# Performance work log

Hardware: AMD Instinct MI355X
Metric: run time of the kernel (lower is better)

Reference implementation:

```python
import jax, jax.numpy as jnp
import numpy as np

WS = 7          # window size
NUM_HEADS = 4
DIM = 128


def setup_inputs() -> dict:
    key = jax.random.key(0)
    k1, k2, k3, k4, k5 = jax.random.split(key, 5)
    B, H, W, C = 16, 112, 112, DIM
    x = jax.random.normal(k1, (B, H, W, C), dtype=jnp.float32)
    w_qkv = jax.random.normal(k2, (C, 3 * C), dtype=jnp.float32) * 0.02
    b_qkv = jax.random.normal(k3, (3 * C,), dtype=jnp.float32) * 0.02
    w_proj = jax.random.normal(k4, (C, C), dtype=jnp.float32) * 0.02
    b_proj = jax.random.normal(k5, (C,), dtype=jnp.float32) * 0.02
    return {"x": x, "w_qkv": w_qkv, "b_qkv": b_qkv, "w_proj": w_proj, "b_proj": b_proj}


def reference(x, w_qkv, b_qkv, w_proj, b_proj):
    B, H, W, C = x.shape
    nh, hd = NUM_HEADS, C // NUM_HEADS
    scale = hd ** (-0.5)
    pad_h = (WS - H % WS) % WS
    pad_w = (WS - W % WS) % WS
    if pad_h > 0 or pad_w > 0:
        x = jnp.pad(x, ((0, 0), (0, pad_h), (0, pad_w), (0, 0)))
    Hp, Wp = H + pad_h, W + pad_w
    nH, nW = Hp // WS, Wp // WS
    # window partition: [B,Hp,Wp,C] -> [B*nH*nW, WS*WS, C]
    win = x.reshape(B, nH, WS, nW, WS, C).transpose(0, 1, 3, 2, 4, 5)
    win = win.reshape(-1, WS * WS, C)
    nwin, N = win.shape[0], WS * WS
    qkv = win @ w_qkv + b_qkv                       # [nwin, N, 3C]
    qkv = qkv.reshape(nwin, N, 3, nh, hd).transpose(2, 0, 3, 1, 4)  # [3, nwin, nh, N, hd]
    q, k, v = qkv[0], qkv[1], qkv[2]
    attn = jnp.einsum("whnd,whmd->whnm", q, k) * scale
    attn = jax.nn.softmax(attn, axis=-1)
    out = jnp.einsum("whnm,whmd->whnd", attn, v)    # [nwin, nh, N, hd]
    out = out.transpose(0, 2, 1, 3).reshape(nwin, N, C)
    out = out @ w_proj + b_proj
    # window merge: [nwin, N, C] -> [B, Hp, Wp, C]
    out = out.reshape(B, nH, nW, WS, WS, C).transpose(0, 1, 3, 2, 4, 5)
    out = out.reshape(B, Hp, Wp, C)
    if pad_h > 0 or pad_w > 0:
        out = out[:, :H, :W, :]
    return out
```

## Files before the change

kernel.cpp:

```cpp
#include <hip/hip_runtime.h>
#include <hip/hip_bf16.h>

typedef short bf16x8 __attribute__((ext_vector_type(8)));
typedef short bf16x4 __attribute__((ext_vector_type(4)));
typedef float f32x4 __attribute__((ext_vector_type(4)));
typedef unsigned short ushort8v __attribute__((ext_vector_type(8)));

#define TPB 512

__device__ __forceinline__ unsigned short f2bf(float f) {
  __hip_bfloat16 h = __float2bfloat16(f);
  return __builtin_bit_cast(unsigned short, h);
}

__device__ __forceinline__ bf16x4 pack4(float a, float b, float c, float d) {
  bf16x4 v;
  v[0] = (short)f2bf(a); v[1] = (short)f2bf(b);
  v[2] = (short)f2bf(c); v[3] = (short)f2bf(d);
  return v;
}

__device__ __forceinline__ f32x4 mfma16(bf16x4 a, bf16x4 b, f32x4 c) {
#if __has_builtin(__builtin_amdgcn_mfma_f32_16x16x16_bf16)
  return __builtin_amdgcn_mfma_f32_16x16x16_bf16(a, b, c, 0, 0, 0);
#elif __has_builtin(__builtin_amdgcn_mfma_f32_16x16x16bf16_1k)
  return __builtin_amdgcn_mfma_f32_16x16x16bf16_1k(a, b, c, 0, 0, 0);
#else
  f32x4 d;
  asm("v_mfma_f32_16x16x16_bf16 %0, %1, %2, %3" : "=v"(d) : "v"(a), "v"(b), "v"(c));
  return d;
#endif
}

__device__ __forceinline__ float exp2_raw(float x) {
#if __has_builtin(__builtin_amdgcn_exp2f)
  return __builtin_amdgcn_exp2f(x);
#else
  float r; asm("v_exp_f32 %0, %1" : "=v"(r) : "v"(x)); return r;
#endif
}
__device__ __forceinline__ float rcp_raw(float x) {
#if __has_builtin(__builtin_amdgcn_rcpf)
  return __builtin_amdgcn_rcpf(x);
#else
  float r; asm("v_rcp_f32 %0, %1" : "=v"(r) : "v"(x)); return r;
#endif
}

#define Q_OFF   0
#define K_OFF   10240
#define ATT_OFF 0
#define VT_OFF  20480
#define SMEM_ELEMS 29696

#define CQ 0.25501817f

__global__ void prep_weights(const float* __restrict__ wqkv,
                             const float* __restrict__ wproj,
                             unsigned short* __restrict__ wt) {
  int idx = blockIdx.x * 256 + threadIdx.x;
  if (idx < 384 * 128) {
    int n = idx >> 7, k = idx & 127;
    wt[idx] = f2bf(wqkv[k * 384 + n]);
  } else if (idx < 384 * 128 + 128 * 128) {
    int j = idx - 384 * 128;
    int c = j >> 7, k = j & 127;
    wt[idx] = f2bf(wproj[k * 128 + c]);
  }
}

__launch_bounds__(TPB, 2)
__global__ void win_attn(const float* __restrict__ x,
                         const float* __restrict__ bqkv,
                         const float* __restrict__ bproj,
                         const unsigned short* __restrict__ wt,
                         float* __restrict__ out) {
  __shared__ __align__(16) unsigned short smem[SMEM_ELEMS];
  const int tid  = threadIdx.x;
  const int wave = tid >> 6;
  const int lane = tid & 63;
  const int g    = lane >> 4;
  const int l15  = lane & 15;

  const int wid = blockIdx.x;
  const int b = wid >> 8, wh = (wid >> 4) & 15, ww = wid & 15;
  const size_t winbase = (((size_t)b * 112 + wh * 7) * 112 + ww * 7) * 128;

  const unsigned short* wqkvT  = wt;
  const unsigned short* wprojT = wt + 384 * 128;

  bf16x4 idQ = {0, 0, 0, 0}, idK = {0, 0, 0, 0};
  if ((l15 >> 2) == g) {
    idQ[l15 & 3] = (short)f2bf(CQ);
    idK[l15 & 3] = (short)0x3F80;
  }

  for (int q = tid; q < 1024; q += TPB) {
    int row = q >> 4, c8 = q & 15;
    int rowc = min(row, 48);
    const float4* src = (const float4*)(x + winbase + ((rowc / 7) * 112 + (rowc % 7)) * 128 + c8 * 8);
    float4 f0 = src[0], f1 = src[1];
    ushort8v v8;
    v8[0] = f2bf(f0.x); v8[1] = f2bf(f0.y); v8[2] = f2bf(f0.z); v8[3] = f2bf(f0.w);
    v8[4] = f2bf(f1.x); v8[5] = f2bf(f1.y); v8[6] = f2bf(f1.z); v8[7] = f2bf(f1.w);
    int dst = row * 128 + ((c8 * 8) ^ ((row & 7) << 3));
    *(ushort8v*)(&smem[dst]) = v8;
  }
  __syncthreads();

  bf16x8 af[4][4];
#pragma unroll
  for (int mt = 0; mt < 4; mt++)
#pragma unroll
    for (int kt = 0; kt < 4; kt++) {
      int row = mt * 16 + l15;
      int colE = kt * 32 + g * 8;
      af[mt][kt] = *(const bf16x8*)(&smem[row * 128 + (colE ^ ((row & 7) << 3))]);
    }
  __syncthreads();

  const f32x4 zero4 = {0.f, 0.f, 0.f, 0.f};

#pragma unroll
  for (int i = 0; i < 3; i++) {
    int nt = wave * 3 + i;
    int n  = nt * 16 + l15;
    float bias = bqkv[n];
    f32x4 binit = {bias, bias, bias, bias};

    bf16x8 bw[4];
#pragma unroll
    for (int kt = 0; kt < 4; kt++)
      bw[kt] = *(const bf16x8*)(wqkvT + n * 128 + kt * 32 + g * 8);

    f32x4 acc[4] = {binit, binit, binit, binit};
    __builtin_amdgcn_s_setprio(1);
#pragma unroll
    for (int kt = 0; kt < 4; kt++)
#pragma unroll
      for (int mt = 0; mt < 4; mt++)
        acc[mt] = __builtin_amdgcn_mfma_f32_16x16x32_bf16(af[mt][kt], bw[kt], acc[mt], 0, 0, 0);
    __builtin_amdgcn_s_setprio(0);

    int sec = nt >> 3;
    if (sec == 2) {
      int hn = n & 127, h = hn >> 5, d = hn & 31;
#pragma unroll
      for (int mt = 0; mt < 4; mt++) {
        bf16x4 pv = pack4(acc[mt][0], acc[mt][1], acc[mt][2], acc[mt][3]);
        *(bf16x4*)(&smem[VT_OFF + h * 2304 + d * 72 + mt * 16 + g * 4]) = pv;
      }
    } else {
      int t7 = nt & 7;
      int hh = t7 >> 1, d0 = (t7 & 1) * 16;
      const bf16x4 idf = (sec == 0) ? idQ : idK;
      const int base = (sec == 0 ? Q_OFF : K_OFF) + hh * 2560 + d0 + g * 4;
#pragma unroll
      for (int mt = 0; mt < 4; mt++) {
        bf16x4 ax = pack4(acc[mt][0], acc[mt][1], acc[mt][2], acc[mt][3]);
        f32x4 dt = mfma16(ax, idf, zero4);
        bf16x4 w = pack4(dt[0], dt[1], dt[2], dt[3]);
        *(bf16x4*)(&smem[base + (mt * 16 + l15) * 40]) = w;
      }
    }
  }
  __syncthreads();

  const int h    = wave >> 1;
  const int half = wave & 1;

  bf16x8 ak[4];
#pragma unroll
  for (int kt = 0; kt < 4; kt++) {
    int row = kt * 16 + l15;
    ak[kt] = *(const bf16x8*)(&smem[K_OFF + h * 2560 + row * 40 + g * 8]);
  }
  bf16x8 bq[2];
#pragma unroll
  for (int qt = 0; qt < 2; qt++) {
    int row = half * 32 + qt * 16 + l15;
    bq[qt] = *(const bf16x8*)(&smem[Q_OFF + h * 2560 + row * 40 + g * 8]);
  }
  bf16x4 bv16[2][4];
#pragma unroll
  for (int nt2 = 0; nt2 < 2; nt2++)
#pragma unroll
    for (int kt = 0; kt < 4; kt++)
      bv16[nt2][kt] = *(const bf16x4*)(&smem[VT_OFF + h * 2304 + (nt2 * 16 + l15) * 72 + kt * 16 + g * 4]);

  f32x4 s[4][2];
  __builtin_amdgcn_s_setprio(1);
#pragma unroll
  for (int kt = 0; kt < 4; kt++)
#pragma unroll
    for (int qt = 0; qt < 2; qt++)
      s[kt][qt] = __builtin_amdgcn_mfma_f32_16x16x32_bf16(ak[kt], bq[qt], zero4, 0, 0, 0);
  __builtin_amdgcn_s_setprio(0);

  bf16x4 ap16[2][4];
  const bool v48 = (g == 0);
#pragma unroll
  for (int qt = 0; qt < 2; qt++) {
    float sum = 0.f;
#pragma unroll
    for (int kt = 0; kt < 3; kt++)
#pragma unroll
      for (int r = 0; r < 4; r++) {
        float p = exp2_raw(s[kt][qt][r]);
        s[kt][qt][r] = p;
        sum += p;
      }
    float p3 = v48 ? exp2_raw(s[3][qt][0]) : 0.0f;
    sum += p3;
    sum += __shfl_xor(sum, 16);
    sum += __shfl_xor(sum, 32);
    float inv = rcp_raw(sum);
#pragma unroll
    for (int kt = 0; kt < 3; kt++)
      ap16[qt][kt] = pack4(s[kt][qt][0] * inv, s[kt][qt][1] * inv,
                           s[kt][qt][2] * inv, s[kt][qt][3] * inv);
    ap16[qt][3] = pack4(p3 * inv, 0.f, 0.f, 0.f);
  }

  f32x4 o[2][2] = {{zero4, zero4}, {zero4, zero4}};
  __builtin_amdgcn_s_setprio(1);
#pragma unroll
  for (int kt = 0; kt < 4; kt++)
#pragma unroll
    for (int m2 = 0; m2 < 2; m2++)
#pragma unroll
      for (int nt2 = 0; nt2 < 2; nt2++)
        o[m2][nt2] = mfma16(ap16[m2][kt], bv16[nt2][kt], o[m2][nt2]);
  __builtin_amdgcn_s_setprio(0);

  bf16x4 attw[2][2];
#pragma unroll
  for (int m2 = 0; m2 < 2; m2++)
#pragma unroll
    for (int nt2 = 0; nt2 < 2; nt2++) {
      bf16x4 ox = pack4(o[m2][nt2][0], o[m2][nt2][1], o[m2][nt2][2], o[m2][nt2][3]);
      f32x4 ot = mfma16(ox, idK, zero4);
      attw[m2][nt2] = pack4(ot[0], ot[1], ot[2], ot[3]);
    }

  const int ccol = wave * 16 + l15;
  bf16x8 bwp[4];
#pragma unroll
  for (int kt = 0; kt < 4; kt++)
    bwp[kt] = *(const bf16x8*)(wprojT + ccol * 128 + kt * 32 + g * 8);
  float biasp = bproj[ccol];

  __syncthreads();

#pragma unroll
  for (int m2 = 0; m2 < 2; m2++)
#pragma unroll
    for (int nt2 = 0; nt2 < 2; nt2++) {
      int tok  = (half * 2 + m2) * 16 + l15;
      int col0 = h * 32 + nt2 * 16 + g * 4;
      *(bf16x4*)(&smem[ATT_OFF + tok * 128 + (col0 ^ ((tok & 7) << 3))]) = attw[m2][nt2];
    }
  __syncthreads();

  f32x4 po[4] = {zero4, zero4, zero4, zero4};
  __builtin_amdgcn_s_setprio(1);
#pragma unroll
  for (int kt = 0; kt < 4; kt++) {
#pragma unroll
    for (int mt = 0; mt < 4; mt++) {
      int row = mt * 16 + l15;
      int colE = kt * 32 + g * 8;
      bf16x8 aa = *(const bf16x8*)(&smem[ATT_OFF + row * 128 + (colE ^ ((row & 7) << 3))]);
      po[mt] = __builtin_amdgcn_mfma_f32_16x16x32_bf16(aa, bwp[kt], po[mt], 0, 0, 0);
    }
  }
  __builtin_amdgcn_s_setprio(0);
#pragma unroll
  for (int mt = 0; mt < 3; mt++)
#pragma unroll
    for (int r = 0; r < 4; r++) {
      int tok = mt * 16 + g * 4 + r;
      size_t off = winbase + ((size_t)(tok / 7) * 112 + (tok % 7)) * 128 + ccol;
      out[off] = po[mt][r] + biasp;
    }
  if (g == 0) {
    size_t off = winbase + ((size_t)6 * 112 + 6) * 128 + ccol;
    out[off] = po[3][0] + biasp;
  }
}

extern "C" void kernel_launch(void* const* d_in, const int* in_sizes, int n_in,
                              void* d_out, int out_size, void* d_ws, size_t ws_size,
                              hipStream_t stream) {
  (void)in_sizes; (void)n_in; (void)out_size; (void)ws_size;
  const float* x     = (const float*)d_in[0];
  const float* wqkv  = (const float*)d_in[1];
  const float* bqkv  = (const float*)d_in[2];
  const float* wproj = (const float*)d_in[3];
  const float* bproj = (const float*)d_in[4];
  unsigned short* wt = (unsigned short*)d_ws;

  hipLaunchKernelGGL(prep_weights, dim3(256), dim3(256), 0, stream, wqkv, wproj, wt);
  hipLaunchKernelGGL(win_attn, dim3(4096), dim3(TPB), 0, stream,
                     x, bqkv, bproj, wt, (float*)d_out);
}
```

Baseline: 95.57 us.

## Make window-attention blocks persistent over 8 windows with register prefetch

Each block now processes 8 windows in a loop instead of one, so the grid shrinks to 512 blocks. The next window's x tile is loaded into registers during the current window's attention stage and written to shared memory after the attention-output stage. To allow this, the attention-output buffer moves to a separate shared-memory region so the prefetched input does not overwrite it. The aim is to hide global load latency and amortise block launch cost. The price is fewer blocks in flight (512 blocks on 256 CUs at 2 per CU), more registers for the prefetch buffers, and an extra barrier per window.

Result: faster. 84.99 us (-11.1%).

```diff
diff --git a/kernel.cpp b/kernel.cpp
--- a/kernel.cpp
+++ b/kernel.cpp
@@ -6,7 +6,8 @@
 typedef float f32x4 __attribute__((ext_vector_type(4)));
 typedef unsigned short ushort8v __attribute__((ext_vector_type(8)));
 
-#define TPB 512
+#define TPB  512
+#define NWIN 8
 
 __device__ __forceinline__ unsigned short f2bf(float f) {
   __hip_bfloat16 h = __float2bfloat16(f);
@@ -49,7 +50,7 @@
 
 #define Q_OFF   0
 #define K_OFF   10240
-#define ATT_OFF 0
+#define ATT_OFF 10240
 #define VT_OFF  20480
 #define SMEM_ELEMS 29696
 
@@ -67,6 +68,11 @@
     int c = j >> 7, k = j & 127;
     wt[idx] = f2bf(wproj[k * 128 + c]);
   }
+}
+
+__device__ __forceinline__ size_t winbase_of(int wid) {
+  int b = wid >> 8, wh = (wid >> 4) & 15, ww = wid & 15;
+  return (((size_t)b * 112 + wh * 7) * 112 + ww * 7) * 128;
 }
 
 __launch_bounds__(TPB, 2)
@@ -82,10 +88,6 @@
   const int g    = lane >> 4;
   const int l15  = lane & 15;
 
-  const int wid = blockIdx.x;
-  const int b = wid >> 8, wh = (wid >> 4) & 15, ww = wid & 15;
-  const size_t winbase = (((size_t)b * 112 + wh * 7) * 112 + ww * 7) * 128;
-
   const unsigned short* wqkvT  = wt;
   const unsigned short* wprojT = wt + 384 * 128;
 
@@ -95,197 +97,230 @@
     idK[l15 & 3] = (short)0x3F80;
   }
 
-  for (int q = tid; q < 1024; q += TPB) {
-    int row = q >> 4, c8 = q & 15;
-    int rowc = min(row, 48);
-    const float4* src = (const float4*)(x + winbase + ((rowc / 7) * 112 + (rowc % 7)) * 128 + c8 * 8);
-    float4 f0 = src[0], f1 = src[1];
-    ushort8v v8;
-    v8[0] = f2bf(f0.x); v8[1] = f2bf(f0.y); v8[2] = f2bf(f0.z); v8[3] = f2bf(f0.w);
-    v8[4] = f2bf(f1.x); v8[5] = f2bf(f1.y); v8[6] = f2bf(f1.z); v8[7] = f2bf(f1.w);
-    int dst = row * 128 + ((c8 * 8) ^ ((row & 7) << 3));
-    *(ushort8v*)(&smem[dst]) = v8;
-  }
-  __syncthreads();
-
-  bf16x8 af[4][4];
-#pragma unroll
-  for (int mt = 0; mt < 4; mt++)
-#pragma unroll
-    for (int kt = 0; kt < 4; kt++) {
-      int row = mt * 16 + l15;
-      int colE = kt * 32 + g * 8;
-      af[mt][kt] = *(const bf16x8*)(&smem[row * 128 + (colE ^ ((row & 7) << 3))]);
-    }
-  __syncthreads();
+  const int row0  = tid >> 4, c8 = tid & 15;
+  const int rowc0 = min(row0, 48), rowc1 = min(row0 + 32, 48);
+  const int xo0   = ((rowc0 / 7) * 112 + (rowc0 % 7)) * 128 + c8 * 8;
+  const int xo1   = ((rowc1 / 7) * 112 + (rowc1 % 7)) * 128 + c8 * 8;
+  const int sw    = (c8 * 8) ^ ((row0 & 7) << 3);
+  const int dst0  = row0 * 128 + sw;
+  const int dst1  = (row0 + 32) * 128 + sw;
 
   const f32x4 zero4 = {0.f, 0.f, 0.f, 0.f};
-
-#pragma unroll
-  for (int i = 0; i < 3; i++) {
-    int nt = wave * 3 + i;
-    int n  = nt * 16 + l15;
-    float bias = bqkv[n];
-    f32x4 binit = {bias, bias, bias, bias};
-
-    bf16x8 bw[4];
-#pragma unroll
-    for (int kt = 0; kt < 4; kt++)
-      bw[kt] = *(const bf16x8*)(wqkvT + n * 128 + kt * 32 + g * 8);
-
-    f32x4 acc[4] = {binit, binit, binit, binit};
-    __builtin_amdgcn_s_setprio(1);
-#pragma unroll
-    for (int kt = 0; kt < 4; kt++)
-#pragma unroll
-      for (int mt = 0; mt < 4; mt++)
-        acc[mt] = __builtin_amdgcn_mfma_f32_16x16x32_bf16(af[mt][kt], bw[kt], acc[mt], 0, 0, 0);
-    __builtin_amdgcn_s_setprio(0);
-
-    int sec = nt >> 3;
-    if (sec == 2) {
-      int hn = n & 127, h = hn >> 5, d = hn & 31;
-#pragma unroll
-      for (int mt = 0; mt < 4; mt++) {
-        bf16x4 pv = pack4(acc[mt][0], acc[mt][1], acc[mt][2], acc[mt][3]);
-        *(bf16x4*)(&smem[VT_OFF + h * 2304 + d * 72 + mt * 16 + g * 4]) = pv;
-      }
-    } else {
-      int t7 = nt & 7;
-      int hh = t7 >> 1, d0 = (t7 & 1) * 16;
-      const bf16x4 idf = (sec == 0) ? idQ : idK;
-      const int base = (sec == 0 ? Q_OFF : K_OFF) + hh * 2560 + d0 + g * 4;
-#pragma unroll
-      for (int mt = 0; mt < 4; mt++) {
-        bf16x4 ax = pack4(acc[mt][0], acc[mt][1], acc[mt][2], acc[mt][3]);
-        f32x4 dt = mfma16(ax, idf, zero4);
-        bf16x4 w = pack4(dt[0], dt[1], dt[2], dt[3]);
-        *(bf16x4*)(&smem[base + (mt * 16 + l15) * 40]) = w;
-      }
-    }
-  }
-  __syncthreads();
-
   const int h    = wave >> 1;
   const int half = wave & 1;
-
-  bf16x8 ak[4];
-#pragma unroll
-  for (int kt = 0; kt < 4; kt++) {
-    int row = kt * 16 + l15;
-    ak[kt] = *(const bf16x8*)(&smem[K_OFF + h * 2560 + row * 40 + g * 8]);
-  }
-  bf16x8 bq[2];
-#pragma unroll
-  for (int qt = 0; qt < 2; qt++) {
-    int row = half * 32 + qt * 16 + l15;
-    bq[qt] = *(const bf16x8*)(&smem[Q_OFF + h * 2560 + row * 40 + g * 8]);
-  }
-  bf16x4 bv16[2][4];
-#pragma unroll
-  for (int nt2 = 0; nt2 < 2; nt2++)
+  const int ccol = wave * 16 + l15;
+
+  float4 pfa, pfb, pfc, pfd;
+  {
+    size_t wb0 = winbase_of((int)blockIdx.x);
+    const float4* s0 = (const float4*)(x + wb0 + xo0);
+    const float4* s1 = (const float4*)(x + wb0 + xo1);
+    pfa = s0[0]; pfb = s0[1]; pfc = s1[0]; pfd = s1[1];
+  }
+  {
+    ushort8v v8;
+    v8[0]=f2bf(pfa.x); v8[1]=f2bf(pfa.y); v8[2]=f2bf(pfa.z); v8[3]=f2bf(pfa.w);
+    v8[4]=f2bf(pfb.x); v8[5]=f2bf(pfb.y); v8[6]=f2bf(pfb.z); v8[7]=f2bf(pfb.w);
+    *(ushort8v*)(&smem[dst0]) = v8;
+    v8[0]=f2bf(pfc.x); v8[1]=f2bf(pfc.y); v8[2]=f2bf(pfc.z); v8[3]=f2bf(pfc.w);
+    v8[4]=f2bf(pfd.x); v8[5]=f2bf(pfd.y); v8[6]=f2bf(pfd.z); v8[7]=f2bf(pfd.w);
+    *(ushort8v*)(&smem[dst1]) = v8;
+  }
+  __syncthreads();
+
+  for (int w = 0; w < NWIN; w++) {
+    const int wid = w * 512 + (int)blockIdx.x;
+    const size_t winbase = winbase_of(wid);
+
+    bf16x8 af[4][4];
+#pragma unroll
+    for (int mt = 0; mt < 4; mt++)
+#pragma unroll
+      for (int kt = 0; kt < 4; kt++) {
+        int row = mt * 16 + l15;
+        int colE = kt * 32 + g * 8;
+        af[mt][kt] = *(const bf16x8*)(&smem[row * 128 + (colE ^ ((row & 7) << 3))]);
+      }
+    __syncthreads();
+
+#pragma unroll
+    for (int i = 0; i < 3; i++) {
+      int nt = wave * 3 + i;
+      int n  = nt * 16 + l15;
+      float bias = bqkv[n];
+      f32x4 binit = {bias, bias, bias, bias};
+
+      bf16x8 bw[4];
+#pragma unroll
+      for (int kt = 0; kt < 4; kt++)
+        bw[kt] = *(const bf16x8*)(wqkvT + n * 128 + kt * 32 + g * 8);
+
+      f32x4 acc[4] = {binit, binit, binit, binit};
+      __builtin_amdgcn_s_setprio(1);
+#pragma unroll
+      for (int kt = 0; kt < 4; kt++)
+#pragma unroll
+        for (int mt = 0; mt < 4; mt++)
+          acc[mt] = __builtin_amdgcn_mfma_f32_16x16x32_bf16(af[mt][kt], bw[kt], acc[mt], 0, 0, 0);
+      __builtin_amdgcn_s_setprio(0);
+
+      int sec = nt >> 3;
+      if (sec == 2) {
+        int hn = n & 127, hh = hn >> 5, d = hn & 31;
+#pragma unroll
+        for (int mt = 0; mt < 4; mt++) {
+          bf16x4 pv = pack4(acc[mt][0], acc[mt][1], acc[mt][2], acc[mt][3]);
+          *(bf16x4*)(&smem[VT_OFF + hh * 2304 + d * 72 + mt * 16 + g * 4]) = pv;
+        }
+      } else {
+        int t7 = nt & 7;
+        int hh = t7 >> 1, d0 = (t7 & 1) * 16;
+        const bf16x4 idf = (sec == 0) ? idQ : idK;
+        const int base = (sec == 0 ? Q_OFF : K_OFF) + hh * 2560 + d0 + g * 4;
+#pragma unroll
+        for (int mt = 0; mt < 4; mt++) {
+          bf16x4 ax = pack4(acc[mt][0], acc[mt][1], acc[mt][2], acc[mt][3]);
+          f32x4 dt = mfma16(ax, idf, zero4);
+          bf16x4 wv = pack4(dt[0], dt[1], dt[2], dt[3]);
+          *(bf16x4*)(&smem[base + (mt * 16 + l15) * 40]) = wv;
+        }
+      }
+    }
+    __syncthreads();
+
+    bf16x8 ak[4];
+#pragma unroll
+    for (int kt = 0; kt < 4; kt++) {
+      int row = kt * 16 + l15;
+      ak[kt] = *(const bf16x8*)(&smem[K_OFF + h * 2560 + row * 40 + g * 8]);
+    }
+    bf16x8 bq[2];
+#pragma unroll
+    for (int qt = 0; qt < 2; qt++) {
+      int row = half * 32 + qt * 16 + l15;
+      bq[qt] = *(const bf16x8*)(&smem[Q_OFF + h * 2560 + row * 40 + g * 8]);
+    }
+    bf16x4 bv16[2][4];
+#pragma unroll
+    for (int nt2 = 0; nt2 < 2; nt2++)
+#pragma unroll
+      for (int kt = 0; kt < 4; kt++)
+        bv16[nt2][kt] = *(const bf16x4*)(&smem[VT_OFF + h * 2304 + (nt2 * 16 + l15) * 72 + kt * 16 + g * 4]);
+
+    f32x4 s[4][2];
+    __builtin_amdgcn_s_setprio(1);
 #pragma unroll
     for (int kt = 0; kt < 4; kt++)
-      bv16[nt2][kt] = *(const bf16x4*)(&smem[VT_OFF + h * 2304 + (nt2 * 16 + l15) * 72 + kt * 16 + g * 4]);
-
-  f32x4 s[4][2];
-  __builtin_amdgcn_s_setprio(1);
-#pragma unroll
-  for (int kt = 0; kt < 4; kt++)
-#pragma unroll
-    for (int qt = 0; qt < 2; qt++)
-      s[kt][qt] = __builtin_amdgcn_mfma_f32_16x16x32_bf16(ak[kt], bq[qt], zero4, 0, 0, 0);
-  __builtin_amdgcn_s_setprio(0);
-
-  bf16x4 ap16[2][4];
-  const bool v48 = (g == 0);
-#pragma unroll
-  for (int qt = 0; qt < 2; qt++) {
-    float sum = 0.f;
-#pragma unroll
-    for (int kt = 0; kt < 3; kt++)
+#pragma unroll
+      for (int qt = 0; qt < 2; qt++)
+        s[kt][qt] = __builtin_amdgcn_mfma_f32_16x16x32_bf16(ak[kt], bq[qt], zero4, 0, 0, 0);
+    __builtin_amdgcn_s_setprio(0);
+
+    bf16x4 ap16[2][4];
+    const bool v48 = (g == 0);
+#pragma unroll
+    for (int qt = 0; qt < 2; qt++) {
+      float sum = 0.f;
+#pragma unroll
+      for (int kt = 0; kt < 3; kt++)
+#pragma unroll
+        for (int r = 0; r < 4; r++) {
+          float p = exp2_raw(s[kt][qt][r]);
+          s[kt][qt][r] = p;
+          sum += p;
+        }
+      float p3 = v48 ? exp2_raw(s[3][qt][0]) : 0.0f;
+      sum += p3;
+      sum += __shfl_xor(sum, 16);
+      sum += __shfl_xor(sum, 32);
+      float inv = rcp_raw(sum);
+#pragma unroll
+      for (int kt = 0; kt < 3; kt++)
+        ap16[qt][kt] = pack4(s[kt][qt][0] * inv, s[kt][qt][1] * inv,
+                             s[kt][qt][2] * inv, s[kt][qt][3] * inv);
+      ap16[qt][3] = pack4(p3 * inv, 0.f, 0.f, 0.f);
+    }
+
+    f32x4 o[2][2] = {{zero4, zero4}, {zero4, zero4}};
+    __builtin_amdgcn_s_setprio(1);
+#pragma unroll
+    for (int kt = 0; kt < 4; kt++)
+#pragma unroll
+      for (int m2 = 0; m2 < 2; m2++)
+#pragma unroll
+        for (int nt2 = 0; nt2 < 2; nt2++)
+          o[m2][nt2] = mfma16(ap16[m2][kt], bv16[nt2][kt], o[m2][nt2]);
+    __builtin_amdgcn_s_setprio(0);
+
+    bf16x4 attw[2][2];
+#pragma unroll
+    for (int m2 = 0; m2 < 2; m2++)
+#pragma unroll
+      for (int nt2 = 0; nt2 < 2; nt2++) {
+        bf16x4 ox = pack4(o[m2][nt2][0], o[m2][nt2][1], o[m2][nt2][2], o[m2][nt2][3]);
+        f32x4 ot = mfma16(ox, idK, zero4);
+        attw[m2][nt2] = pack4(ot[0], ot[1], ot[2], ot[3]);
+      }
+
+    if (w < NWIN - 1) {
+      size_t wbn = winbase_of(wid + 512);
+      const float4* s0 = (const float4*)(x + wbn + xo0);
+      const float4* s1 = (const float4*)(x + wbn + xo1);
+      pfa = s0[0]; pfb = s0[1]; pfc = s1[0]; pfd = s1[1];
+    }
+
+    bf16x8 bwp[4];
+#pragma unroll
+    for (int kt = 0; kt < 4; kt++)
+      bwp[kt] = *(const bf16x8*)(wprojT + ccol * 128 + kt * 32 + g * 8);
+    float biasp = bproj[ccol];
+
+    __syncthreads();
+
+#pragma unroll
+    for (int m2 = 0; m2 < 2; m2++)
+#pragma unroll
+      for (int nt2 = 0; nt2 < 2; nt2++) {
+        int tok  = (half * 2 + m2) * 16 + l15;
+        int col0 = h * 32 + nt2 * 16 + g * 4;
+        *(bf16x4*)(&smem[ATT_OFF + tok * 128 + (col0 ^ ((tok & 7) << 3))]) = attw[m2][nt2];
+      }
+    if (w < NWIN - 1) {
+      ushort8v v8;
+      v8[0]=f2bf(pfa.x); v8[1]=f2bf(pfa.y); v8[2]=f2bf(pfa.z); v8[3]=f2bf(pfa.w);
+      v8[4]=f2bf(pfb.x); v8[5]=f2bf(pfb.y); v8[6]=f2bf(pfb.z); v8[7]=f2bf(pfb.w);
+      *(ushort8v*)(&smem[dst0]) = v8;
+      v8[0]=f2bf(pfc.x); v8[1]=f2bf(pfc.y); v8[2]=f2bf(pfc.z); v8[3]=f2bf(pfc.w);
+      v8[4]=f2bf(pfd.x); v8[5]=f2bf(pfd.y); v8[6]=f2bf(pfd.z); v8[7]=f2bf(pfd.w);
+      *(ushort8v*)(&smem[dst1]) = v8;
+    }
+    __syncthreads();
+
+    f32x4 po[4] = {zero4, zero4, zero4, zero4};
+    __builtin_amdgcn_s_setprio(1);
+#pragma unroll
+    for (int kt = 0; kt < 4; kt++) {
+#pragma unroll
+      for (int mt = 0; mt < 4; mt++) {
+        int row = mt * 16 + l15;
+        int colE = kt * 32 + g * 8;
+        bf16x8 aa = *(const bf16x8*)(&smem[ATT_OFF + row * 128 + (colE ^ ((row & 7) << 3))]);
+        po[mt] = __builtin_amdgcn_mfma_f32_16x16x32_bf16(aa, bwp[kt], po[mt], 0, 0, 0);
+      }
+    }
+    __builtin_amdgcn_s_setprio(0);
+#pragma unroll
+    for (int mt = 0; mt < 3; mt++)
 #pragma unroll
       for (int r = 0; r < 4; r++) {
-        float p = exp2_raw(s[kt][qt][r]);
-        s[kt][qt][r] = p;
-        sum += p;
-      }
-    float p3 = v48 ? exp2_raw(s[3][qt][0]) : 0.0f;
-    sum += p3;
-    sum += __shfl_xor(sum, 16);
-    sum += __shfl_xor(sum, 32);
-    float inv = rcp_raw(sum);
-#pragma unroll
-    for (int kt = 0; kt < 3; kt++)
-      ap16[qt][kt] = pack4(s[kt][qt][0] * inv, s[kt][qt][1] * inv,
-                           s[kt][qt][2] * inv, s[kt][qt][3] * inv);
-    ap16[qt][3] = pack4(p3 * inv, 0.f, 0.f, 0.f);
-  }
-
-  f32x4 o[2][2] = {{zero4, zero4}, {zero4, zero4}};
-  __builtin_amdgcn_s_setprio(1);
-#pragma unroll
-  for (int kt = 0; kt < 4; kt++)
-#pragma unroll
-    for (int m2 = 0; m2 < 2; m2++)
-#pragma unroll
-      for (int nt2 = 0; nt2 < 2; nt2++)
-        o[m2][nt2] = mfma16(ap16[m2][kt], bv16[nt2][kt], o[m2][nt2]);
-  __builtin_amdgcn_s_setprio(0);
-
-  bf16x4 attw[2][2];
-#pragma unroll
-  for (int m2 = 0; m2 < 2; m2++)
-#pragma unroll
-    for (int nt2 = 0; nt2 < 2; nt2++) {
-      bf16x4 ox = pack4(o[m2][nt2][0], o[m2][nt2][1], o[m2][nt2][2], o[m2][nt2][3]);
-      f32x4 ot = mfma16(ox, idK, zero4);
-      attw[m2][nt2] = pack4(ot[0], ot[1], ot[2], ot[3]);
-    }
-
-  const int ccol = wave * 16 + l15;
-  bf16x8 bwp[4];
-#pragma unroll
-  for (int kt = 0; kt < 4; kt++)
-    bwp[kt] = *(const bf16x8*)(wprojT + ccol * 128 + kt * 32 + g * 8);
-  float biasp = bproj[ccol];
-
-  __syncthreads();
-
-#pragma unroll
-  for (int m2 = 0; m2 < 2; m2++)
-#pragma unroll
-    for (int nt2 = 0; nt2 < 2; nt2++) {
-      int tok  = (half * 2 + m2) * 16 + l15;
-      int col0 = h * 32 + nt2 * 16 + g * 4;
-      *(bf16x4*)(&smem[ATT_OFF + tok * 128 + (col0 ^ ((tok & 7) << 3))]) = attw[m2][nt2];
-    }
-  __syncthreads();
-
-  f32x4 po[4] = {zero4, zero4, zero4, zero4};
-  __builtin_amdgcn_s_setprio(1);
-#pragma unroll
-  for (int kt = 0; kt < 4; kt++) {
-#pragma unroll
-    for (int mt = 0; mt < 4; mt++) {
-      int row = mt * 16 + l15;
-      int colE = kt * 32 + g * 8;
-      bf16x8 aa = *(const bf16x8*)(&smem[ATT_OFF + row * 128 + (colE ^ ((row & 7) << 3))]);
-      po[mt] = __builtin_amdgcn_mfma_f32_16x16x32_bf16(aa, bwp[kt], po[mt], 0, 0, 0);
-    }
-  }
-  __builtin_amdgcn_s_setprio(0);
-#pragma unroll
-  for (int mt = 0; mt < 3; mt++)
-#pragma unroll
-    for (int r = 0; r < 4; r++) {
-      int tok = mt * 16 + g * 4 + r;
-      size_t off = winbase + ((size_t)(tok / 7) * 112 + (tok % 7)) * 128 + ccol;
-      out[off] = po[mt][r] + biasp;
-    }
-  if (g == 0) {
-    size_t off = winbase + ((size_t)6 * 112 + 6) * 128 + ccol;
-    out[off] = po[3][0] + biasp;
+        int tok = mt * 16 + g * 4 + r;
+        size_t off = winbase + ((size_t)(tok / 7) * 112 + (tok % 7)) * 128 + ccol;
+        out[off] = po[mt][r] + biasp;
+      }
+    if (g == 0) {
+      size_t off = winbase + ((size_t)6 * 112 + 6) * 128 + ccol;
+      out[off] = po[3][0] + biasp;
+    }
   }
 }
 
@@ -301,6 +336,6 @@
   unsigned short* wt = (unsigned short*)d_ws;
 
   hipLaunchKernelGGL(prep_weights, dim3(256), dim3(256), 0, stream, wqkv, wproj, wt);
-  hipLaunchKernelGGL(win_attn, dim3(4096), dim3(TPB), 0, stream,
+  hipLaunchKernelGGL(win_attn, dim3(4096 / NWIN), dim3(TPB), 0, stream,
                      x, bqkv, bproj, wt, (float*)d_out);
 }
```
